# Optimization experiments

Measured on AMD Instinct MI355X. Metric: run time of the kernel, lower is better.

## Reference

```python
import jax, jax.numpy as jnp
import numpy as np

D_MODEL = 1024
N_HEADS = 16
HEAD_DIM = D_MODEL // N_HEADS
SCALE = HEAD_DIM ** -0.5
MASK_FILL = -10000.0


def setup_inputs() -> dict:
    key = jax.random.key(0)
    ks = jax.random.split(key, 12)
    B, L, D = 2, 2048, D_MODEL
    inv = 1.0 / np.sqrt(D)
    inp = {
        "query": jax.random.normal(ks[0], (B, L, D), jnp.float32),
        "key": jax.random.normal(ks[1], (B, L, D), jnp.float32),
        "value": jax.random.normal(ks[2], (B, L, D), jnp.float32),
        "Wq": jax.random.normal(ks[3], (D, D), jnp.float32) * inv,
        "bq": jnp.zeros((D,), jnp.float32),
        "Wk": jax.random.normal(ks[4], (D, D), jnp.float32) * inv,
        "bk": jnp.zeros((D,), jnp.float32),
        "Wv": jax.random.normal(ks[5], (D, D), jnp.float32) * inv,
        "bv": jnp.zeros((D,), jnp.float32),
        "Wo": jax.random.normal(ks[6], (D, D), jnp.float32) * inv,
        "bo": jnp.zeros((D,), jnp.float32),
        "valid_mask": jax.random.randint(ks[7], (B, L), 0, 2).astype(jnp.bool_),
    }
    return inp


def reference(query, key, value, Wq, bq, Wk, bk, Wv, bv, Wo, bo, valid_mask):
    B, Lq, D = query.shape
    Lk = key.shape[1]
    H, HD = N_HEADS, HEAD_DIM
    # torch.nn.Linear: y = x @ W.T + b
    Q = (query @ Wq.T + bq).reshape(B, Lq, H, HD).transpose(0, 2, 1, 3)  # [B,H,Lq,HD]
    K = (key @ Wk.T + bk).reshape(B, Lk, H, HD).transpose(0, 2, 1, 3)    # [B,H,Lk,HD]
    V = (value @ Wv.T + bv).reshape(B, Lk, H, HD).transpose(0, 2, 1, 3)  # [B,H,Lk,HD]
    scores = jnp.einsum("bhqd,bhkd->bhqk", Q, K) * SCALE
    scores = jnp.where(valid_mask[:, None, None, :], scores, MASK_FILL)
    weights = jax.nn.softmax(scores, axis=-1)  # dropout is identity at inference
    out = jnp.einsum("bhqk,bhkd->bhqd", weights, V)
    out = out.transpose(0, 2, 1, 3).reshape(B, Lq, D)
    out = out @ Wo.T + bo
    # zero rows of fully-invalid batches
    gate = jnp.any(valid_mask, axis=1).astype(out.dtype)[:, None, None]
    return out * gate
```

## Files before the change

### kernel.cpp

```cpp
#include <hip/hip_runtime.h>
#include <hip/hip_bf16.h>

typedef __hip_bfloat16 bf16;
typedef __attribute__((ext_vector_type(8))) short s8v;
typedef __attribute__((ext_vector_type(4))) float f4v;

#define LOG2E 1.44269504088896340736f
#define CSCALE (0.125f * LOG2E)
#define MASK_B2 (-14426.950408889634f)

#define BB 2
#define LL 2048
#define DD 1024
#define HH 16
#define HD 64
#define MTOT 4096
#define PER_T 4194304

struct alignas(8) B4 { bf16 v[4]; };

__device__ __forceinline__ void async_cp16(const bf16* g, bf16* l) {
    __builtin_amdgcn_global_load_lds(
        (const __attribute__((address_space(1))) void*)g,
        (__attribute__((address_space(3))) void*)l, 16, 0, 0);
}

struct CvtArgs {
    const float* src[7];
    bf16* dst[7];
    int n[7];
};

__global__ __launch_bounds__(256) void cvt_kernel(CvtArgs args) {
    const int which = blockIdx.y;
    const float* __restrict__ src = args.src[which];
    bf16* __restrict__ dst = args.dst[which];
    const int n4 = args.n[which] >> 2;
    const int stride = gridDim.x * 256;
    for (int i = blockIdx.x * 256 + threadIdx.x; i < n4; i += stride) {
        const float4 f = ((const float4*)src)[i];
        B4 o;
        o.v[0] = __float2bfloat16(f.x);
        o.v[1] = __float2bfloat16(f.y);
        o.v[2] = __float2bfloat16(f.z);
        o.v[3] = __float2bfloat16(f.w);
        ((B4*)dst)[i] = o;
    }
}

struct QkvArgs {
    const bf16* A[3];
    const bf16* W[3];
    const float* bias[3];
    bf16* out[3];
};

template <int FUSED, int SWAP>
__device__ __forceinline__ void gemm_body(const bf16* __restrict__ A,
                                          const bf16* __restrict__ W,
                                          const float* __restrict__ bias,
                                          bf16* __restrict__ out_bf,
                                          float* __restrict__ out_f,
                                          float gatef, char* smem) {
    bf16* sA = (bf16*)smem;
    bf16* sB = (bf16*)(smem + 128 * 64 * 2);
    bf16* sE = (bf16*)smem;

    const int lane = threadIdx.x & 63;
    const int w = threadIdx.x >> 6;
    const int lr = lane & 15;
    const int quad = lane >> 4;
    const int wr = w >> 1, wc = w & 1;
    const int rbase = blockIdx.x * 128;
    const int cbase = blockIdx.y * 128;
    const int dma_r = lane >> 3;
    const int dma_cc = ((lane & 7) ^ dma_r) * 8;

    f4v acc[4][4] = {};
    for (int kt = 0; kt < DD / 64; kt++) {
        const int k0 = kt * 64;
        __syncthreads();
#pragma unroll
        for (int t = 0; t < 4; t++) {
            const int g = w * 4 + t;
            async_cp16(A + (size_t)(rbase + g * 8 + dma_r) * DD + k0 + dma_cc,
                       &sA[g * 512]);
            async_cp16(W + (size_t)(cbase + g * 8 + dma_r) * DD + k0 + dma_cc,
                       &sB[g * 512]);
        }
        __syncthreads();
#pragma unroll
        for (int s = 0; s < 2; s++) {
            s8v a[4], b[4];
#pragma unroll
            for (int i = 0; i < 4; i++) {
                const int row = wr * 64 + i * 16 + lr;
                a[i] = *(const s8v*)&sA[row * 64 + (((s * 4 + quad) ^ (row & 7)) * 8)];
            }
#pragma unroll
            for (int j = 0; j < 4; j++) {
                const int row = wc * 64 + j * 16 + lr;
                b[j] = *(const s8v*)&sB[row * 64 + (((s * 4 + quad) ^ (row & 7)) * 8)];
            }
#pragma unroll
            for (int i = 0; i < 4; i++)
#pragma unroll
                for (int j = 0; j < 4; j++)
                    acc[i][j] = SWAP
                        ? __builtin_amdgcn_mfma_f32_16x16x32_bf16(b[j], a[i], acc[i][j], 0, 0, 0)
                        : __builtin_amdgcn_mfma_f32_16x16x32_bf16(a[i], b[j], acc[i][j], 0, 0, 0);
        }
    }
    __syncthreads();

    if (FUSED == 0) {
#pragma unroll
        for (int j = 0; j < 4; j++) {
            const int n = cbase + wc * 64 + j * 16 + quad * 4;
            const f4v bv = *(const f4v*)&bias[n];
#pragma unroll
            for (int i = 0; i < 4; i++) {
                const int m = rbase + wr * 64 + i * 16 + lr;
                float4 o;
                o.x = (acc[i][j][0] + bv[0]) * gatef;
                o.y = (acc[i][j][1] + bv[1]) * gatef;
                o.z = (acc[i][j][2] + bv[2]) * gatef;
                o.w = (acc[i][j][3] + bv[3]) * gatef;
                *(float4*)&out_f[(size_t)m * DD + n] = o;
            }
        }
        return;
    }

    if (SWAP) {
#pragma unroll
        for (int j = 0; j < 4; j++) {
            const int n_loc = wc * 64 + j * 16 + quad * 4;
            const f4v bv = *(const f4v*)&bias[cbase + n_loc];
#pragma unroll
            for (int i = 0; i < 4; i++) {
                const int m_loc = wr * 64 + i * 16 + lr;
                B4 pk;
                pk.v[0] = __float2bfloat16(acc[i][j][0] + bv[0]);
                pk.v[1] = __float2bfloat16(acc[i][j][1] + bv[1]);
                pk.v[2] = __float2bfloat16(acc[i][j][2] + bv[2]);
                pk.v[3] = __float2bfloat16(acc[i][j][3] + bv[3]);
                *(B4*)&sE[m_loc * 136 + n_loc] = pk;
            }
        }
        __syncthreads();
        const int tid = threadIdx.x;
        const int mr_ = tid >> 4;
        const int n0 = (tid & 15) * 8;
#pragma unroll
        for (int ro = 0; ro < 8; ro++) {
            const int m_loc = ro * 16 + mr_;
            const s8v vv = *(const s8v*)&sE[m_loc * 136 + n0];
            const int m = rbase + m_loc;
            const int n = cbase + n0;
            const int b_ = m >> 11, l = m & (LL - 1);
            const int h = n >> 6, hd = n & 63;
            *(s8v*)&out_bf[(((size_t)(b_ * HH + h)) * LL + l) * HD + hd] = vv;
        }
    } else {
#pragma unroll
        for (int j = 0; j < 4; j++) {
            const int n_loc = wc * 64 + j * 16 + lr;
            const float bv = bias[cbase + n_loc];
#pragma unroll
            for (int i = 0; i < 4; i++) {
                const int m0 = wr * 64 + i * 16 + quad * 4;
                B4 pk;
                pk.v[0] = __float2bfloat16(acc[i][j][0] + bv);
                pk.v[1] = __float2bfloat16(acc[i][j][1] + bv);
                pk.v[2] = __float2bfloat16(acc[i][j][2] + bv);
                pk.v[3] = __float2bfloat16(acc[i][j][3] + bv);
                *(B4*)&sE[n_loc * 136 + m0] = pk;
            }
        }
        __syncthreads();
        const int tid = threadIdx.x;
#pragma unroll
        for (int ro = 0; ro < 8; ro++) {
            const int n_loc = ro * 16 + (tid >> 4);
            const int m0 = (tid & 15) * 8;
            const s8v vv = *(const s8v*)&sE[n_loc * 136 + m0];
            const int n = cbase + n_loc;
            const int m = rbase + m0;
            const int b_ = m >> 11, l = m & (LL - 1);
            const int h = n >> 6, hd = n & 63;
            *(s8v*)&out_bf[(((size_t)(b_ * HH + h)) * HD + hd) * LL + l] = vv;
        }
    }
}

template <int FUSED>
__global__ __launch_bounds__(256) void gemm128(QkvArgs qa,
                                               const bf16* __restrict__ Ao,
                                               const bf16* __restrict__ Wo_,
                                               const float* __restrict__ bo_,
                                               float* __restrict__ out_f,
                                               const int* __restrict__ mask) {
    __shared__ __align__(16) char smem[128 * 136 * 2];
    __shared__ int sgate;

    float gatef = 1.0f;
    if (!FUSED) {
        if (threadIdx.x == 0) sgate = 0;
        __syncthreads();
        const int b_ = (int)(blockIdx.x * 128) >> 11;
        int any = 0;
        for (int i = threadIdx.x; i < LL; i += 256) any |= mask[b_ * LL + i];
        if (any) sgate = 1;
        __syncthreads();
        gatef = sgate ? 1.0f : 0.0f;
    }

    if (FUSED) {
        const int which = blockIdx.z;
        if (which != 2)
            gemm_body<1, 1>(qa.A[which], qa.W[which], qa.bias[which],
                            qa.out[which], nullptr, 1.0f, smem);
        else
            gemm_body<1, 0>(qa.A[2], qa.W[2], qa.bias[2],
                            qa.out[2], nullptr, 1.0f, smem);
    } else {
        gemm_body<0, 1>(Ao, Wo_, bo_, nullptr, out_f, gatef, smem);
    }
}

__global__ __launch_bounds__(512) void attn_kernel(const bf16* __restrict__ Q,
                                                   const bf16* __restrict__ K,
                                                   const bf16* __restrict__ Vt,
                                                   const int* __restrict__ mask,
                                                   bf16* __restrict__ Aout) {
    __shared__ bf16 sK[2][64 * 64];
    __shared__ bf16 sV[2][64 * 64];
    __shared__ float sBias[LL];

    const int lane = threadIdx.x & 63;
    const int w = threadIdx.x >> 6;
    const int lr = lane & 15;
    const int quad = lane >> 4;

    const int bid = blockIdx.x;
    const int qb = bid & 15;
    const int h = (bid >> 4) & 15;
    const int b = bid >> 8;

    const size_t head_off = ((size_t)(b * HH + h)) * LL * HD;
    const bf16* Qh = Q + head_off;
    const bf16* Kh = K + head_off;
    const bf16* Vh = Vt + head_off;
    const int q0 = qb * 128 + w * 16;

    const int dma_r = lane >> 3;
    const int dma_cv = ((lane & 7) ^ dma_r) * 8;
    const int dma_ck = ((lane & 7) ^ ((dma_r & 3) | ((w & 1) << 2))) * 8;

    {
        const int* mb = mask + b * LL;
        for (int i = threadIdx.x; i < LL; i += 512)
            sBias[i] = mb[i] ? 0.0f : MASK_B2;
        async_cp16(Kh + (size_t)(w * 8 + dma_r) * HD + dma_ck, &sK[0][w * 512]);
        async_cp16(Vh + (size_t)(w * 8 + dma_r) * LL + dma_cv, &sV[0][w * 512]);
    }
    __syncthreads();

    const s8v aq0 = *(const s8v*)(Qh + (size_t)(q0 + lr) * HD + quad * 8);
    const s8v aq1 = *(const s8v*)(Qh + (size_t)(q0 + lr) * HD + 32 + quad * 8);

    f4v O[4] = {};
    float lacc = 0.0f;

    const int swk = (lr & 3) | (((lr >> 2) & 1) << 2);
    const int swv = lr & 7;
    const int krow0 = 8 * (lr >> 2) + (lr & 3);

    for (int kt = 0; kt < LL / 64; kt++) {
        const int kbase = kt * 64;
        const bf16* kb = &sK[kt & 1][0];
        const bf16* vb = &sV[kt & 1][0];

        if (kt < LL / 64 - 1) {
            const int nb = (kt + 1) & 1;
            async_cp16(Kh + (size_t)(kbase + 64 + w * 8 + dma_r) * HD + dma_ck,
                       &sK[nb][w * 512]);
            async_cp16(Vh + (size_t)(w * 8 + dma_r) * LL + kbase + 64 + dma_cv,
                       &sV[nb][w * 512]);
        }

        f4v T[4];
        __builtin_amdgcn_s_setprio(1);
#pragma unroll
        for (int j = 0; j < 4; j++) {
            const int row = krow0 + 32 * (j >> 1) + 4 * (j & 1);
            const s8v kb0 = *(const s8v*)&kb[row * 64 + ((quad ^ swk) * 8)];
            const s8v kb1 = *(const s8v*)&kb[row * 64 + (((quad + 4) ^ swk) * 8)];
            f4v t = {};
            t = __builtin_amdgcn_mfma_f32_16x16x32_bf16(kb0, aq0, t, 0, 0, 0);
            T[j] = __builtin_amdgcn_mfma_f32_16x16x32_bf16(kb1, aq1, t, 0, 0, 0);
        }
        __builtin_amdgcn_s_setprio(0);

        s8v v0[4], v1[4];
#pragma unroll
        for (int dt = 0; dt < 4; dt++) {
            const int vrow = dt * 16 + lr;
            v0[dt] = *(const s8v*)&vb[vrow * 64 + ((quad ^ swv) * 8)];
            v1[dt] = *(const s8v*)&vb[vrow * 64 + (((quad + 4) ^ swv) * 8)];
        }

        union { s8v v; bf16 e[8]; } p0, p1;
#pragma unroll
        for (int j = 0; j < 4; j++) {
            const f4v bj = *(const f4v*)&sBias[kbase + 32 * (j >> 1) + 8 * quad + 4 * (j & 1)];
#pragma unroll
            for (int r = 0; r < 4; r++) {
                const float e = exp2f(T[j][r] * CSCALE + bj[r]);
                T[j][r] = e;
                lacc += e;
            }
        }
#pragma unroll
        for (int r = 0; r < 4; r++) {
            p0.e[r]     = __float2bfloat16(T[0][r]);
            p0.e[r + 4] = __float2bfloat16(T[1][r]);
            p1.e[r]     = __float2bfloat16(T[2][r]);
            p1.e[r + 4] = __float2bfloat16(T[3][r]);
        }

        __builtin_amdgcn_s_setprio(1);
#pragma unroll
        for (int dt = 0; dt < 4; dt++) {
            O[dt] = __builtin_amdgcn_mfma_f32_16x16x32_bf16(v0[dt], p0.v, O[dt], 0, 0, 0);
            O[dt] = __builtin_amdgcn_mfma_f32_16x16x32_bf16(v1[dt], p1.v, O[dt], 0, 0, 0);
        }
        __builtin_amdgcn_s_setprio(0);

        __syncthreads();
    }

    float lt = lacc;
    lt += __shfl_xor(lt, 16);
    lt += __shfl_xor(lt, 32);
    const float linv = (lt > 0.0f) ? (1.0f / lt) : 0.0f;

#pragma unroll
    for (int dt = 0; dt < 4; dt++) {
        B4 o;
#pragma unroll
        for (int r = 0; r < 4; r++) o.v[r] = __float2bfloat16(O[dt][r] * linv);
        *(B4*)&Aout[((size_t)(b * LL + q0 + lr)) * DD + h * HD + dt * 16 + quad * 4] = o;
    }
}

extern "C" void kernel_launch(void* const* d_in, const int* in_sizes, int n_in,
                              void* d_out, int out_size, void* d_ws, size_t ws_size,
                              hipStream_t stream) {
    const float* query = (const float*)d_in[0];
    const float* key   = (const float*)d_in[1];
    const float* value = (const float*)d_in[2];
    const float* Wq = (const float*)d_in[3];
    const float* bq = (const float*)d_in[4];
    const float* Wk = (const float*)d_in[5];
    const float* bk = (const float*)d_in[6];
    const float* Wv = (const float*)d_in[7];
    const float* bv = (const float*)d_in[8];
    const float* Wo = (const float*)d_in[9];
    const float* bo = (const float*)d_in[10];
    const int* mask = (const int*)d_in[11];

    bf16* base = (bf16*)d_ws;
    bf16* qx = base;
    bf16* kx = qx + PER_T;
    bf16* vx = kx + PER_T;
    bf16* wq = vx + PER_T;
    bf16* wk = wq + DD * DD;
    bf16* wv = wk + DD * DD;
    bf16* wo = wv + DD * DD;
    bf16* Qs = wo + DD * DD;
    bf16* Ks = Qs + PER_T;
    bf16* Vst = Ks + PER_T;
    bf16* aws = Vst + PER_T;

    CvtArgs ca;
    ca.src[0] = query; ca.dst[0] = qx; ca.n[0] = PER_T;
    ca.src[1] = key;   ca.dst[1] = kx; ca.n[1] = PER_T;
    ca.src[2] = value; ca.dst[2] = vx; ca.n[2] = PER_T;
    ca.src[3] = Wq;    ca.dst[3] = wq; ca.n[3] = DD * DD;
    ca.src[4] = Wk;    ca.dst[4] = wk; ca.n[4] = DD * DD;
    ca.src[5] = Wv;    ca.dst[5] = wv; ca.n[5] = DD * DD;
    ca.src[6] = Wo;    ca.dst[6] = wo; ca.n[6] = DD * DD;
    cvt_kernel<<<dim3(1024, 7), 256, 0, stream>>>(ca);

    QkvArgs qa;
    qa.A[0] = qx; qa.W[0] = wq; qa.bias[0] = bq; qa.out[0] = Qs;
    qa.A[1] = kx; qa.W[1] = wk; qa.bias[1] = bk; qa.out[1] = Ks;
    qa.A[2] = vx; qa.W[2] = wv; qa.bias[2] = bv; qa.out[2] = Vst;

    gemm128<1><<<dim3(MTOT / 128, DD / 128, 3), 256, 0, stream>>>(
        qa, nullptr, nullptr, nullptr, nullptr, nullptr);

    attn_kernel<<<BB * HH * (LL / 128), 512, 0, stream>>>(Qs, Ks, Vst, mask, aws);

    QkvArgs dummy{};
    gemm128<0><<<dim3(MTOT / 128, DD / 128, 1), 256, 0, stream>>>(
        dummy, aws, wo, bo, (float*)d_out, mask);
}
```

Before: 244.7 us.

## Fuse fp32-to-bf16 activation conversion into QKV GEMM tile loads

Drops the separate conversion pass over the query/key/value activations. The QKV GEMM now reads fp32 activations directly with register loads, converts them to bf16 and writes them into the swizzled shared-memory tile. Only the weights still go through the standalone convert kernel. This removes a full write and reread of about 48MB of bf16 intermediates. In exchange, the A-tile load becomes synchronous register traffic instead of async global-to-LDS copies, and each activation element is reread by every column block.

```diff
diff --git a/kernel.cpp b/kernel.cpp
--- a/kernel.cpp
+++ b/kernel.cpp
@@ -26,9 +26,9 @@
 }
 
 struct CvtArgs {
-    const float* src[7];
-    bf16* dst[7];
-    int n[7];
+    const float* src[4];
+    bf16* dst[4];
+    int n[4];
 };
 
 __global__ __launch_bounds__(256) void cvt_kernel(CvtArgs args) {
@@ -49,14 +49,14 @@
 }
 
 struct QkvArgs {
-    const bf16* A[3];
+    const float* A[3];
     const bf16* W[3];
     const float* bias[3];
     bf16* out[3];
 };
 
-template <int FUSED, int SWAP>
-__device__ __forceinline__ void gemm_body(const bf16* __restrict__ A,
+template <int FUSED, int SWAP, int AF32>
+__device__ __forceinline__ void gemm_body(const void* Aptr,
                                           const bf16* __restrict__ W,
                                           const float* __restrict__ bias,
                                           bf16* __restrict__ out_bf,
@@ -65,6 +65,9 @@
     bf16* sA = (bf16*)smem;
     bf16* sB = (bf16*)(smem + 128 * 64 * 2);
     bf16* sE = (bf16*)smem;
+
+    const bf16* __restrict__ Ab = (const bf16*)Aptr;
+    const float* __restrict__ Af = (const float*)Aptr;
 
     const int lane = threadIdx.x & 63;
     const int w = threadIdx.x >> 6;
@@ -83,10 +86,33 @@
 #pragma unroll
         for (int t = 0; t < 4; t++) {
             const int g = w * 4 + t;
-            async_cp16(A + (size_t)(rbase + g * 8 + dma_r) * DD + k0 + dma_cc,
-                       &sA[g * 512]);
             async_cp16(W + (size_t)(cbase + g * 8 + dma_r) * DD + k0 + dma_cc,
                        &sB[g * 512]);
+            if (!AF32)
+                async_cp16(Ab + (size_t)(rbase + g * 8 + dma_r) * DD + k0 + dma_cc,
+                           &sA[g * 512]);
+        }
+        if (AF32) {
+#pragma unroll
+            for (int t = 0; t < 4; t++) {
+                const int g = w * 4 + t;
+#pragma unroll
+                for (int i = 0; i < 2; i++) {
+                    const int li = lane + i * 64;
+                    const int row = li >> 4;
+                    const int fcol = (li & 15) * 4;
+                    const float4 f = *(const float4*)&Af[
+                        (size_t)(rbase + g * 8 + row) * DD + k0 + fcol];
+                    B4 pk;
+                    pk.v[0] = __float2bfloat16(f.x);
+                    pk.v[1] = __float2bfloat16(f.y);
+                    pk.v[2] = __float2bfloat16(f.z);
+                    pk.v[3] = __float2bfloat16(f.w);
+                    const int chunk = fcol >> 3;
+                    *(B4*)&sA[g * 512 + row * 64 + ((chunk ^ row) & 7) * 8 +
+                              (fcol & 7)] = pk;
+                }
+            }
         }
         __syncthreads();
 #pragma unroll
@@ -219,13 +245,13 @@
     if (FUSED) {
         const int which = blockIdx.z;
         if (which != 2)
-            gemm_body<1, 1>(qa.A[which], qa.W[which], qa.bias[which],
-                            qa.out[which], nullptr, 1.0f, smem);
+            gemm_body<1, 1, 1>(qa.A[which], qa.W[which], qa.bias[which],
+                               qa.out[which], nullptr, 1.0f, smem);
         else
-            gemm_body<1, 0>(qa.A[2], qa.W[2], qa.bias[2],
-                            qa.out[2], nullptr, 1.0f, smem);
+            gemm_body<1, 0, 1>(qa.A[2], qa.W[2], qa.bias[2],
+                               qa.out[2], nullptr, 1.0f, smem);
     } else {
-        gemm_body<0, 1>(Ao, Wo_, bo_, nullptr, out_f, gatef, smem);
+        gemm_body<0, 1, 0>(Ao, Wo_, bo_, nullptr, out_f, gatef, smem);
     }
 }
 
@@ -372,10 +398,7 @@
     const int* mask = (const int*)d_in[11];
 
     bf16* base = (bf16*)d_ws;
-    bf16* qx = base;
-    bf16* kx = qx + PER_T;
-    bf16* vx = kx + PER_T;
-    bf16* wq = vx + PER_T;
+    bf16* wq = base;
     bf16* wk = wq + DD * DD;
     bf16* wv = wk + DD * DD;
     bf16* wo = wv + DD * DD;
@@ -385,19 +408,16 @@
     bf16* aws = Vst + PER_T;
 
     CvtArgs ca;
-    ca.src[0] = query; ca.dst[0] = qx; ca.n[0] = PER_T;
-    ca.src[1] = key;   ca.dst[1] = kx; ca.n[1] = PER_T;
-    ca.src[2] = value; ca.dst[2] = vx; ca.n[2] = PER_T;
-    ca.src[3] = Wq;    ca.dst[3] = wq; ca.n[3] = DD * DD;
-    ca.src[4] = Wk;    ca.dst[4] = wk; ca.n[4] = DD * DD;
-    ca.src[5] = Wv;    ca.dst[5] = wv; ca.n[5] = DD * DD;
-    ca.src[6] = Wo;    ca.dst[6] = wo; ca.n[6] = DD * DD;
-    cvt_kernel<<<dim3(1024, 7), 256, 0, stream>>>(ca);
+    ca.src[0] = Wq; ca.dst[0] = wq; ca.n[0] = DD * DD;
+    ca.src[1] = Wk; ca.dst[1] = wk; ca.n[1] = DD * DD;
+    ca.src[2] = Wv; ca.dst[2] = wv; ca.n[2] = DD * DD;
+    ca.src[3] = Wo; ca.dst[3] = wo; ca.n[3] = DD * DD;
+    cvt_kernel<<<dim3(256, 4), 256, 0, stream>>>(ca);
 
     QkvArgs qa;
-    qa.A[0] = qx; qa.W[0] = wq; qa.bias[0] = bq; qa.out[0] = Qs;
-    qa.A[1] = kx; qa.W[1] = wk; qa.bias[1] = bk; qa.out[1] = Ks;
-    qa.A[2] = vx; qa.W[2] = wv; qa.bias[2] = bv; qa.out[2] = Vst;
+    qa.A[0] = query; qa.W[0] = wq; qa.bias[0] = bq; qa.out[0] = Qs;
+    qa.A[1] = key;   qa.W[1] = wk; qa.bias[1] = bk; qa.out[1] = Ks;
+    qa.A[2] = value; qa.W[2] = wv; qa.bias[2] = bv; qa.out[2] = Vst;
 
     gemm128<1><<<dim3(MTOT / 128, DD / 128, 3), 256, 0, stream>>>(
         qa, nullptr, nullptr, nullptr, nullptr, nullptr);
```

Result: slower. 254.6 us (+4.1%).
